# Kernel tuning notes

Measured on AMD Instinct MI355X. Metric: run time of the kernel, lower is better.

Reference implementation:

```python
import jax, jax.numpy as jnp
import numpy as np

GROUPS = 32
EPS = 1e-6


def group_norm(x, scale, bias):
    # x: [b,h,w,c] channels-last, 32 groups
    b, h, w, c = x.shape
    g = GROUPS
    xg = x.reshape(b, h, w, g, c // g)
    mean = xg.mean(axis=(1, 2, 4), keepdims=True)
    var = xg.var(axis=(1, 2, 4), keepdims=True)
    xg = (xg - mean) * jax.lax.rsqrt(var + EPS)
    return xg.reshape(b, h, w, c) * scale + bias


def setup_inputs() -> dict:
    key = jax.random.key(0)
    ks = jax.random.split(key, 10)
    b, h, w, c = 8, 64, 64, 256
    x = jax.random.normal(ks[0], (b, h, w, c), dtype=jnp.float32)
    s = 1.0 / np.sqrt(c)
    return {
        "x": x,
        "gn_scale": jnp.ones((c,), jnp.float32),
        "gn_bias": jnp.zeros((c,), jnp.float32),
        "wq": jax.random.normal(ks[1], (c, c), jnp.float32) * s,
        "bq": jnp.zeros((c,), jnp.float32),
        "wk": jax.random.normal(ks[2], (c, c), jnp.float32) * s,
        "bk": jnp.zeros((c,), jnp.float32),
        "wv": jax.random.normal(ks[3], (c, c), jnp.float32) * s,
        "bv": jnp.zeros((c,), jnp.float32),
        "wp": jax.random.normal(ks[4], (c, c), jnp.float32) * s,
        "bp": jnp.zeros((c,), jnp.float32),
    }


def reference(x, gn_scale, gn_bias, wq, bq, wk, bk, wv, bv, wp, bp):
    b, h, w, c = x.shape
    h_ = group_norm(x, gn_scale, gn_bias)
    # 1x1 convs == per-pixel channel matmuls
    q = jnp.einsum('bhwc,cd->bhwd', h_, wq) + bq
    k = jnp.einsum('bhwc,cd->bhwd', h_, wk) + bk
    v = jnp.einsum('bhwc,cd->bhwd', h_, wv) + bv
    q = q.reshape(b, h * w, c)
    k = k.reshape(b, h * w, c)
    v = v.reshape(b, h * w, c)
    scores = jnp.einsum('bqc,bkc->bqk', q, k) * (c ** -0.5)  # [b, hw, hw]
    attn = jax.nn.softmax(scores, axis=2)
    out = jnp.einsum('bqk,bkc->bqc', attn, v).reshape(b, h, w, c)
    out = jnp.einsum('bhwc,cd->bhwd', out, wp) + bp
    return x + out
```

## Files before the change

kernel.cpp:

```cpp
#include <hip/hip_runtime.h>
#include <hip/hip_bf16.h>
#include <stdint.h>

static constexpr int HW = 4096;
static constexpr int Cc = 256;
static constexpr int Gg = 32;
static constexpr float EPSV = 1e-6f;
static constexpr float QSCALE = 0.0625f * 1.44269504f;

typedef __attribute__((ext_vector_type(8))) short bf8_t;
typedef __attribute__((ext_vector_type(4))) float f4_t;
typedef __attribute__((ext_vector_type(16))) float f32x16;

__device__ __forceinline__ ushort f2bf(float x) {
    union { float f; uint32_t u; } v; v.f = x;
    uint32_t r = v.u + 0x7FFFu + ((v.u >> 16) & 1u);
    return (ushort)(r >> 16);
}
__device__ __forceinline__ float bf2f(ushort u) {
    union { uint32_t u; float f; } v; v.u = ((uint32_t)u) << 16;
    return v.f;
}
__device__ __forceinline__ uint32_t cvtpk(float lo, float hi_) {
    uint32_t r;
    asm volatile("v_cvt_pk_bf16_f32 %0, %1, %2" : "=v"(r) : "v"(lo), "v"(hi_));
    return r;
}
__device__ __forceinline__ float fexp2(float x) {
    float r;
    asm("v_exp_f32 %0, %1" : "=v"(r) : "v"(x));
    return r;
}

__device__ __forceinline__ void gload16(const void* g, void* l) {
    __builtin_amdgcn_global_load_lds((const __attribute__((address_space(1))) void*)g,
                                     (__attribute__((address_space(3))) void*)l, 16, 0, 0);
}

__global__ void prep_kernel(const float* __restrict__ x, float* __restrict__ psum,
                            float* __restrict__ psumsq,
                            const float* __restrict__ wq, const float* __restrict__ wk,
                            const float* __restrict__ wv, const float* __restrict__ wp,
                            ushort* __restrict__ wT) {
    int bx = blockIdx.x;
    if (bx < 512) {
        int slice = bx & 63;
        int b = bx >> 6;
        int c = threadIdx.x;
        const float* xp = x + ((size_t)b * HW + (size_t)slice * 64) * Cc + c;
        float s = 0.f, sq = 0.f;
        for (int p = 0; p < 64; ++p) { float v = xp[(size_t)p * Cc]; s += v; sq += v * v; }
        for (int m = 1; m < 8; m <<= 1) { s += __shfl_xor(s, m); sq += __shfl_xor(sq, m); }
        if ((c & 7) == 0) {
            int g = c >> 3;
            psum[(b * Gg + g) * 64 + slice] = s;
            psumsq[(b * Gg + g) * 64 + slice] = sq;
        }
    } else {
        int base = (bx - 512) * 1024 + threadIdx.x * 4;
        int which = base >> 16;
        const float* w = which == 0 ? wq : which == 1 ? wk : which == 2 ? wv : wp;
        int rem = base & 65535;
        int d = rem >> 8, c = rem & 255;
        ushort4 o;
        o.x = f2bf(w[(c + 0) * 256 + d]);
        o.y = f2bf(w[(c + 1) * 256 + d]);
        o.z = f2bf(w[(c + 2) * 256 + d]);
        o.w = f2bf(w[(c + 3) * 256 + d]);
        *(ushort4*)&wT[which * 65536 + d * 256 + c] = o;
    }
}

__global__ void gn_stats(const float* __restrict__ psum, const float* __restrict__ psumsq,
                         float* __restrict__ stats) {
    int t = threadIdx.x;
    float s = 0.f, sq = 0.f;
    for (int i = 0; i < 64; ++i) { s += psum[t * 64 + i]; sq += psumsq[t * 64 + i]; }
    float mean = s * (1.0f / 32768.0f);
    float var = sq * (1.0f / 32768.0f) - mean * mean;
    stats[t * 2] = mean;
    stats[t * 2 + 1] = rsqrtf(var + EPSV);
}

__global__ __launch_bounds__(256) void qkv_gn(const float* __restrict__ x, const float* __restrict__ stats,
                                              const float* __restrict__ gs, const float* __restrict__ gb,
                                              const ushort* __restrict__ wT,
                                              const float* __restrict__ bq, const float* __restrict__ bk,
                                              const float* __restrict__ bv,
                                              ushort* __restrict__ q, ushort* __restrict__ k,
                                              ushort* __restrict__ vT) {
    int lane = threadIdx.x & 63, wvi = threadIdx.x >> 6;
    int lq = lane & 15, lg = lane >> 4;
    int nf0 = wvi * 4;
    int m0b = blockIdx.x * 64;

    bf8_t a[4][8];
#pragma unroll
    for (int tt = 0; tt < 4; ++tt) {
        int row = m0b + tt * 16 + lq;
        int batch = row >> 12;
        const float* xr = x + (size_t)row * 256;
#pragma unroll
        for (int ks = 0; ks < 8; ++ks) {
            int c0 = ks * 32 + lg * 8;
            int g = c0 >> 3;
            float2 st = *(const float2*)&stats[(batch * Gg + g) * 2];
            float4 v0 = *(const float4*)&xr[c0];
            float4 v1 = *(const float4*)&xr[c0 + 4];
            float4 s0 = *(const float4*)&gs[c0];
            float4 s1 = *(const float4*)&gs[c0 + 4];
            float4 b0 = *(const float4*)&gb[c0];
            float4 b1 = *(const float4*)&gb[c0 + 4];
            bf8_t fr;
            fr[0] = (short)f2bf((v0.x - st.x) * st.y * s0.x + b0.x);
            fr[1] = (short)f2bf((v0.y - st.x) * st.y * s0.y + b0.y);
            fr[2] = (short)f2bf((v0.z - st.x) * st.y * s0.z + b0.z);
            fr[3] = (short)f2bf((v0.w - st.x) * st.y * s0.w + b0.w);
            fr[4] = (short)f2bf((v1.x - st.x) * st.y * s1.x + b1.x);
            fr[5] = (short)f2bf((v1.y - st.x) * st.y * s1.y + b1.y);
            fr[6] = (short)f2bf((v1.z - st.x) * st.y * s1.z + b1.z);
            fr[7] = (short)f2bf((v1.w - st.x) * st.y * s1.w + b1.w);
            a[tt][ks] = fr;
        }
    }

#pragma unroll
    for (int which = 0; which < 3; ++which) {
        const ushort* w = wT + which * 65536;
        const float* bias = which == 0 ? bq : which == 1 ? bk : bv;

        f4_t acc[4][4];
#pragma unroll
        for (int tt = 0; tt < 4; ++tt)
#pragma unroll
            for (int i = 0; i < 4; ++i) acc[tt][i] = (f4_t)0.f;

        const ushort* brow = w + (size_t)(nf0 * 16 + lq) * 256 + lg * 8;
#pragma unroll
        for (int nf = 0; nf < 4; ++nf) {
#pragma unroll
            for (int ks = 0; ks < 8; ++ks) {
                bf8_t bfr = *(const bf8_t*)(brow + nf * 16 * 256 + ks * 32);
                acc[0][nf] = __builtin_amdgcn_mfma_f32_16x16x32_bf16(a[0][ks], bfr, acc[0][nf], 0, 0, 0);
                acc[1][nf] = __builtin_amdgcn_mfma_f32_16x16x32_bf16(a[1][ks], bfr, acc[1][nf], 0, 0, 0);
                acc[2][nf] = __builtin_amdgcn_mfma_f32_16x16x32_bf16(a[2][ks], bfr, acc[2][nf], 0, 0, 0);
                acc[3][nf] = __builtin_amdgcn_mfma_f32_16x16x32_bf16(a[3][ks], bfr, acc[3][nf], 0, 0, 0);
            }
        }
#pragma unroll
        for (int tt = 0; tt < 4; ++tt) {
            int m0 = m0b + tt * 16;
            if (which == 2) {
                int bt = m0 >> 12;
                int hw0 = (m0 & 4095) + lg * 4;
#pragma unroll
                for (int nf = 0; nf < 4; ++nf) {
                    int col = (nf0 + nf) * 16 + lq;
                    float bsv = bias[col];
                    ushort4 pk;
                    pk.x = f2bf(acc[tt][nf][0] + bsv);
                    pk.y = f2bf(acc[tt][nf][1] + bsv);
                    pk.z = f2bf(acc[tt][nf][2] + bsv);
                    pk.w = f2bf(acc[tt][nf][3] + bsv);
                    *(ushort4*)&vT[(size_t)bt * (256 * 4096) + (size_t)col * 4096 + hw0] = pk;
                }
            } else {
                ushort* out = which == 0 ? q : k;
                float scale = which == 0 ? QSCALE : 1.0f;
#pragma unroll
                for (int nf = 0; nf < 4; ++nf) {
                    int col = (nf0 + nf) * 16 + lq;
                    float bsv = bias[col];
#pragma unroll
                    for (int r = 0; r < 4; ++r) {
                        int rr = m0 + lg * 4 + r;
                        out[(size_t)rr * 256 + col] = f2bf((acc[tt][nf][r] + bsv) * scale);
                    }
                }
            }
        }
    }
}

__global__ __launch_bounds__(512, 2) void flash_kernel(const ushort* __restrict__ q,
                                                       const ushort* __restrict__ kk,
                                                       const ushort* __restrict__ vT,
                                                       ushort* __restrict__ Opart,
                                                       float* __restrict__ ml) {
    extern __shared__ char smem[];
    const int t = threadIdx.x, lane = t & 63, wvi = t >> 6;
    const int l31 = lane & 31, hi = lane >> 5;
    const int bid = blockIdx.x;
    const int batch = bid & 7, half = (bid >> 3) & 1, qt = bid >> 4;
    const size_t bb = (size_t)batch * HW * Cc;
    const int t0 = half * 32;

    const int qbase = qt * 256 + wvi * 32;
    bf8_t qf[16];
    {
        const ushort* qrow = q + bb + (size_t)(qbase + l31) * Cc + hi * 8;
#pragma unroll
        for (int ks = 0; ks < 16; ++ks) qf[ks] = *(const bf8_t*)(qrow + ks * 16);
    }

    f32x16 o[8];
#pragma unroll
    for (int i = 0; i < 8; ++i) o[i] = (f32x16)0.f;
    float l_i = 0.f;

    const ushort* ksrc_b = kk + bb;
    const ushort* vsrc_b = vT + (size_t)batch * (256 * 4096);
    const int tb = wvi * 64;

    auto stage = [&](int kt, int bufsel) {
        const ushort* ks_ = ksrc_b + (size_t)kt * 64 * 256;
        const ushort* vs_ = vsrc_b + kt * 64;
        char* kd = smem + bufsel * 32768;
        char* vd = smem + 65536 + bufsel * 32768;
#pragma unroll
        for (int i = 0; i < 4; ++i) {
            int n = i * 512 + tb + lane;
            int kr = n >> 5;
            int c = (n & 31) ^ (kr & 7);
            gload16(ks_ + kr * 256 + c * 8, kd + (i * 512 + tb) * 16);
        }
#pragma unroll
        for (int i = 0; i < 4; ++i) {
            int n = i * 512 + tb + lane;
            int d = n >> 3;
            int c = (n & 7) ^ (d & 7);
            gload16(vs_ + (size_t)d * HW + c * 8, vd + (i * 512 + tb) * 16);
        }
    };

    stage(t0, 0);
    asm volatile("s_waitcnt vmcnt(0)" ::: "memory");
    __builtin_amdgcn_s_barrier();
    __builtin_amdgcn_sched_barrier(0);

    for (int it = 0; it < 32; ++it) {
        const int cur = it & 1;
        if (it + 1 < 32) stage(t0 + it + 1, cur ^ 1);

        const char* Kb = smem + cur * 32768;
        const char* Vb = smem + 65536 + cur * 32768;

        f32x16 sa0 = (f32x16)(-8.0f), sa1 = (f32x16)(-8.0f);
        __builtin_amdgcn_s_setprio(1);
#pragma unroll
        for (int ks = 0; ks < 16; ++ks) {
            int chunk = 2 * ks + hi;
            int sw = (chunk ^ (l31 & 7)) * 16;
            bf8_t kf0 = *(const bf8_t*)(Kb + l31 * 512 + sw);
            bf8_t kf1 = *(const bf8_t*)(Kb + (32 + l31) * 512 + sw);
            sa0 = __builtin_amdgcn_mfma_f32_32x32x16_bf16(kf0, qf[ks], sa0, 0, 0, 0);
            sa1 = __builtin_amdgcn_mfma_f32_32x32x16_bf16(kf1, qf[ks], sa1, 0, 0, 0);
        }
        __builtin_amdgcn_s_setprio(0);

#pragma unroll
        for (int s = 0; s < 4; ++s) {
            int b8 = (s & 1) * 8;
            float p0, p1, p2, p3, p4, p5, p6, p7;
            if (s < 2) {
                p0 = fexp2(sa0[b8 + 0]); p1 = fexp2(sa0[b8 + 1]);
                p2 = fexp2(sa0[b8 + 2]); p3 = fexp2(sa0[b8 + 3]);
                p4 = fexp2(sa0[b8 + 4]); p5 = fexp2(sa0[b8 + 5]);
                p6 = fexp2(sa0[b8 + 6]); p7 = fexp2(sa0[b8 + 7]);
            } else {
                p0 = fexp2(sa1[b8 + 0]); p1 = fexp2(sa1[b8 + 1]);
                p2 = fexp2(sa1[b8 + 2]); p3 = fexp2(sa1[b8 + 3]);
                p4 = fexp2(sa1[b8 + 4]); p5 = fexp2(sa1[b8 + 5]);
                p6 = fexp2(sa1[b8 + 6]); p7 = fexp2(sa1[b8 + 7]);
            }
            l_i += ((p0 + p1) + (p2 + p3)) + ((p4 + p5) + (p6 + p7));
            uint32_t w0 = cvtpk(p0, p1), w1 = cvtpk(p2, p3);
            uint32_t w2 = cvtpk(p4, p5), w3 = cvtpk(p6, p7);
            asm volatile("v_permlane32_swap_b32 %0, %1" : "+v"(w0), "+v"(w2));
            asm volatile("v_permlane32_swap_b32 %0, %1" : "+v"(w1), "+v"(w3));
            union { uint32_t u[4]; bf8_t v; } pa;
            pa.u[0] = w0; pa.u[1] = w1; pa.u[2] = w2; pa.u[3] = w3;

            __builtin_amdgcn_s_setprio(1);
#pragma unroll
            for (int nt = 0; nt < 8; ++nt) {
                int d = nt * 32 + l31;
                int ch = 2 * s + hi;
                bf8_t vf = *(const bf8_t*)(Vb + d * 128 + ((ch ^ (d & 7)) * 16));
                o[nt] = __builtin_amdgcn_mfma_f32_32x32x16_bf16(pa.v, vf, o[nt], 0, 0, 0);
            }
            __builtin_amdgcn_s_setprio(0);
        }

        if (it + 1 < 32) {
            asm volatile("s_waitcnt vmcnt(0)" ::: "memory");
            __builtin_amdgcn_s_barrier();
            __builtin_amdgcn_sched_barrier(0);
        }
    }

    float l_row = l_i + __shfl_xor(l_i, 32);
    ushort* op = Opart + (size_t)bid * (256 * 256) + (size_t)(wvi * 32) * 256;
#pragma unroll
    for (int nt = 0; nt < 8; ++nt) {
#pragma unroll
        for (int r = 0; r < 16; ++r) {
            int qrow = (r & 3) + 8 * (r >> 2) + 4 * hi;
            op[(size_t)qrow * 256 + nt * 32 + l31] = f2bf(o[nt][r]);
        }
    }
    if (lane < 32) {
        ml[(size_t)bid * 256 + wvi * 32 + l31] = l_row;
    }
}

__global__ __launch_bounds__(256) void projc_gemm(const ushort* __restrict__ Opart,
                                                  const float* __restrict__ ml,
                                                  const ushort* __restrict__ wT,
                                                  const float* __restrict__ bp,
                                                  const float* __restrict__ x,
                                                  float* __restrict__ outp) {
    int lane = threadIdx.x & 63, wvi = threadIdx.x >> 6;
    int lq = lane & 15, lg = lane >> 4;
    int rowhalf = wvi >> 1, nf0 = (wvi & 1) * 8;
    int m0b = blockIdx.x * 64 + rowhalf * 32;

    bf8_t a[2][8];
#pragma unroll
    for (int tt = 0; tt < 2; ++tt) {
        int row = m0b + tt * 16 + lq;
        int batch = row >> 12, rr = row & 4095;
        int qt = rr >> 8, rit = rr & 255;
        int blkA = batch + 16 * qt, blkB = blkA + 8;
        float la = ml[(size_t)blkA * 256 + rit];
        float lb = ml[(size_t)blkB * 256 + rit];
        float inv = 1.0f / (la + lb);
        const ushort* Arow = Opart + (size_t)blkA * 65536 + (size_t)rit * 256 + lg * 8;
        const ushort* Brow = Opart + (size_t)blkB * 65536 + (size_t)rit * 256 + lg * 8;
#pragma unroll
        for (int ks = 0; ks < 8; ++ks) {
            bf8_t fa = *(const bf8_t*)(Arow + ks * 32);
            bf8_t fb = *(const bf8_t*)(Brow + ks * 32);
            bf8_t mg;
#pragma unroll
            for (int j = 0; j < 8; ++j)
                mg[j] = (short)f2bf((bf2f((ushort)fa[j]) + bf2f((ushort)fb[j])) * inv);
            a[tt][ks] = mg;
        }
    }

    f4_t acc[2][8];
#pragma unroll
    for (int tt = 0; tt < 2; ++tt)
#pragma unroll
        for (int i = 0; i < 8; ++i) acc[tt][i] = (f4_t)0.f;

    const ushort* brow = wT + (size_t)(nf0 * 16 + lq) * 256 + lg * 8;
#pragma unroll
    for (int nf = 0; nf < 8; ++nf) {
#pragma unroll
        for (int ks = 0; ks < 8; ++ks) {
            bf8_t bfr = *(const bf8_t*)(brow + nf * 16 * 256 + ks * 32);
            acc[0][nf] = __builtin_amdgcn_mfma_f32_16x16x32_bf16(a[0][ks], bfr, acc[0][nf], 0, 0, 0);
            acc[1][nf] = __builtin_amdgcn_mfma_f32_16x16x32_bf16(a[1][ks], bfr, acc[1][nf], 0, 0, 0);
        }
    }
#pragma unroll
    for (int tt = 0; tt < 2; ++tt) {
#pragma unroll
        for (int nf = 0; nf < 8; ++nf) {
            int col = (nf0 + nf) * 16 + lq;
            float bsv = bp[col];
#pragma unroll
            for (int r = 0; r < 4; ++r) {
                size_t idx = (size_t)(m0b + tt * 16 + lg * 4 + r) * 256 + col;
                outp[idx] = x[idx] + acc[tt][nf][r] + bsv;
            }
        }
    }
}

extern "C" void kernel_launch(void* const* d_in, const int* in_sizes, int n_in,
                              void* d_out, int out_size, void* d_ws, size_t ws_size,
                              hipStream_t stream) {
    const float* x  = (const float*)d_in[0];
    const float* gs = (const float*)d_in[1];
    const float* gb = (const float*)d_in[2];
    const float* wq = (const float*)d_in[3];
    const float* bq = (const float*)d_in[4];
    const float* wk = (const float*)d_in[5];
    const float* bk = (const float*)d_in[6];
    const float* wv = (const float*)d_in[7];
    const float* bv = (const float*)d_in[8];
    const float* wp = (const float*)d_in[9];
    const float* bp = (const float*)d_in[10];
    float* out = (float*)d_out;

    char* ws = (char*)d_ws;
    ushort* wT    = (ushort*)ws;
    float*  psum  = (float*)(ws + 512 * 1024);
    float*  psumsq= (float*)(ws + 576 * 1024);
    float*  stats = (float*)(ws + 640 * 1024);
    ushort* qb    = (ushort*)(ws + (size_t)17 * (1 << 20));
    ushort* kb    = (ushort*)(ws + (size_t)33 * (1 << 20));
    ushort* vTb   = (ushort*)(ws + (size_t)49 * (1 << 20));
    ushort* Opart = (ushort*)(ws + (size_t)65 * (1 << 20));
    float*  mlb   = (float*)(ws + (size_t)97 * (1 << 20));

    prep_kernel<<<768, 256, 0, stream>>>(x, psum, psumsq, wq, wk, wv, wp, wT);
    gn_stats<<<1, 256, 0, stream>>>(psum, psumsq, stats);
    qkv_gn<<<512, 256, 0, stream>>>(x, stats, gs, gb, wT, bq, bk, bv, qb, kb, vTb);

    hipFuncSetAttribute(reinterpret_cast<const void*>(flash_kernel),
                        hipFuncAttributeMaxDynamicSharedMemorySize, 131072);
    flash_kernel<<<256, 512, 131072, stream>>>(qb, kb, vTb, Opart, mlb);

    projc_gemm<<<512, 256, 0, stream>>>(Opart, mlb, wT + 3 * 65536, bp, x, out);
}
```

Measured before the change: 257.7 us.

## Shrink flash attention tiles to 128 query rows and 32-key stages

Restructures the flash kernel from 512-thread blocks with 256 query rows and 64-key tiles to 256-thread blocks with 128 query rows and 32-key tiles. The grid doubles to 512 blocks and LDS per block halves to 64KB, so more blocks can be resident per CU and the grid covers the device more evenly. The LDS swizzles and the projection kernel's indexing change to match the new partial-output layout. In exchange each K/V tile is reused by fewer query rows, so global and LDS traffic grows, and twice as many loop iterations each pay a barrier.

Result: no change. 253.0 us (-1.9%).

```diff
diff --git a/kernel.cpp b/kernel.cpp
--- a/kernel.cpp
+++ b/kernel.cpp
@@ -182,7 +182,7 @@
     }
 }
 
-__global__ __launch_bounds__(512, 2) void flash_kernel(const ushort* __restrict__ q,
+__global__ __launch_bounds__(256, 2) void flash_kernel(const ushort* __restrict__ q,
                                                        const ushort* __restrict__ kk,
                                                        const ushort* __restrict__ vT,
                                                        ushort* __restrict__ Opart,
@@ -193,9 +193,9 @@
     const int bid = blockIdx.x;
     const int batch = bid & 7, half = (bid >> 3) & 1, qt = bid >> 4;
     const size_t bb = (size_t)batch * HW * Cc;
-    const int t0 = half * 32;
-
-    const int qbase = qt * 256 + wvi * 32;
+    const int t0 = half * 64;
+
+    const int qbase = qt * 128 + wvi * 32;
     bf8_t qf[16];
     {
         const ushort* qrow = q + bb + (size_t)(qbase + l31) * Cc + hi * 8;
@@ -210,26 +210,25 @@
 
     const ushort* ksrc_b = kk + bb;
     const ushort* vsrc_b = vT + (size_t)batch * (256 * 4096);
-    const int tb = wvi * 64;
 
     auto stage = [&](int kt, int bufsel) {
-        const ushort* ks_ = ksrc_b + (size_t)kt * 64 * 256;
-        const ushort* vs_ = vsrc_b + kt * 64;
-        char* kd = smem + bufsel * 32768;
-        char* vd = smem + 65536 + bufsel * 32768;
+        const ushort* ks_ = ksrc_b + (size_t)kt * 32 * 256;
+        const ushort* vs_ = vsrc_b + kt * 32;
+        char* kd = smem + bufsel * 16384;
+        char* vd = smem + 32768 + bufsel * 16384;
 #pragma unroll
         for (int i = 0; i < 4; ++i) {
-            int n = i * 512 + tb + lane;
+            int n = i * 256 + t;
             int kr = n >> 5;
             int c = (n & 31) ^ (kr & 7);
-            gload16(ks_ + kr * 256 + c * 8, kd + (i * 512 + tb) * 16);
+            gload16(ks_ + kr * 256 + c * 8, kd + n * 16);
         }
 #pragma unroll
         for (int i = 0; i < 4; ++i) {
-            int n = i * 512 + tb + lane;
-            int d = n >> 3;
-            int c = (n & 7) ^ (d & 7);
-            gload16(vs_ + (size_t)d * HW + c * 8, vd + (i * 512 + tb) * 16);
+            int n = i * 256 + t;
+            int d = n >> 2;
+            int c = (n & 3) ^ (d & 3);
+            gload16(vs_ + (size_t)d * HW + c * 8, vd + n * 16);
         }
     };
 
@@ -238,41 +237,31 @@
     __builtin_amdgcn_s_barrier();
     __builtin_amdgcn_sched_barrier(0);
 
-    for (int it = 0; it < 32; ++it) {
+    for (int it = 0; it < 64; ++it) {
         const int cur = it & 1;
-        if (it + 1 < 32) stage(t0 + it + 1, cur ^ 1);
-
-        const char* Kb = smem + cur * 32768;
-        const char* Vb = smem + 65536 + cur * 32768;
-
-        f32x16 sa0 = (f32x16)(-8.0f), sa1 = (f32x16)(-8.0f);
+        if (it + 1 < 64) stage(t0 + it + 1, cur ^ 1);
+
+        const char* Kb = smem + cur * 16384;
+        const char* Vb = smem + 32768 + cur * 16384;
+
+        f32x16 sa = (f32x16)(-8.0f);
         __builtin_amdgcn_s_setprio(1);
 #pragma unroll
         for (int ks = 0; ks < 16; ++ks) {
             int chunk = 2 * ks + hi;
             int sw = (chunk ^ (l31 & 7)) * 16;
-            bf8_t kf0 = *(const bf8_t*)(Kb + l31 * 512 + sw);
-            bf8_t kf1 = *(const bf8_t*)(Kb + (32 + l31) * 512 + sw);
-            sa0 = __builtin_amdgcn_mfma_f32_32x32x16_bf16(kf0, qf[ks], sa0, 0, 0, 0);
-            sa1 = __builtin_amdgcn_mfma_f32_32x32x16_bf16(kf1, qf[ks], sa1, 0, 0, 0);
+            bf8_t kf = *(const bf8_t*)(Kb + l31 * 512 + sw);
+            sa = __builtin_amdgcn_mfma_f32_32x32x16_bf16(kf, qf[ks], sa, 0, 0, 0);
         }
         __builtin_amdgcn_s_setprio(0);
 
 #pragma unroll
-        for (int s = 0; s < 4; ++s) {
-            int b8 = (s & 1) * 8;
-            float p0, p1, p2, p3, p4, p5, p6, p7;
-            if (s < 2) {
-                p0 = fexp2(sa0[b8 + 0]); p1 = fexp2(sa0[b8 + 1]);
-                p2 = fexp2(sa0[b8 + 2]); p3 = fexp2(sa0[b8 + 3]);
-                p4 = fexp2(sa0[b8 + 4]); p5 = fexp2(sa0[b8 + 5]);
-                p6 = fexp2(sa0[b8 + 6]); p7 = fexp2(sa0[b8 + 7]);
-            } else {
-                p0 = fexp2(sa1[b8 + 0]); p1 = fexp2(sa1[b8 + 1]);
-                p2 = fexp2(sa1[b8 + 2]); p3 = fexp2(sa1[b8 + 3]);
-                p4 = fexp2(sa1[b8 + 4]); p5 = fexp2(sa1[b8 + 5]);
-                p6 = fexp2(sa1[b8 + 6]); p7 = fexp2(sa1[b8 + 7]);
-            }
+        for (int s = 0; s < 2; ++s) {
+            int b8 = s * 8;
+            float p0 = fexp2(sa[b8 + 0]), p1 = fexp2(sa[b8 + 1]);
+            float p2 = fexp2(sa[b8 + 2]), p3 = fexp2(sa[b8 + 3]);
+            float p4 = fexp2(sa[b8 + 4]), p5 = fexp2(sa[b8 + 5]);
+            float p6 = fexp2(sa[b8 + 6]), p7 = fexp2(sa[b8 + 7]);
             l_i += ((p0 + p1) + (p2 + p3)) + ((p4 + p5) + (p6 + p7));
             uint32_t w0 = cvtpk(p0, p1), w1 = cvtpk(p2, p3);
             uint32_t w2 = cvtpk(p4, p5), w3 = cvtpk(p6, p7);
@@ -286,13 +275,13 @@
             for (int nt = 0; nt < 8; ++nt) {
                 int d = nt * 32 + l31;
                 int ch = 2 * s + hi;
-                bf8_t vf = *(const bf8_t*)(Vb + d * 128 + ((ch ^ (d & 7)) * 16));
+                bf8_t vf = *(const bf8_t*)(Vb + d * 64 + ((ch ^ (d & 3)) * 16));
                 o[nt] = __builtin_amdgcn_mfma_f32_32x32x16_bf16(pa.v, vf, o[nt], 0, 0, 0);
             }
             __builtin_amdgcn_s_setprio(0);
         }
 
-        if (it + 1 < 32) {
+        if (it + 1 < 64) {
             asm volatile("s_waitcnt vmcnt(0)" ::: "memory");
             __builtin_amdgcn_s_barrier();
             __builtin_amdgcn_sched_barrier(0);
@@ -300,7 +289,7 @@
     }
 
     float l_row = l_i + __shfl_xor(l_i, 32);
-    ushort* op = Opart + (size_t)bid * (256 * 256) + (size_t)(wvi * 32) * 256;
+    ushort* op = Opart + (size_t)bid * (128 * 256) + (size_t)(wvi * 32) * 256;
 #pragma unroll
     for (int nt = 0; nt < 8; ++nt) {
 #pragma unroll
@@ -310,7 +299,7 @@
         }
     }
     if (lane < 32) {
-        ml[(size_t)bid * 256 + wvi * 32 + l31] = l_row;
+        ml[(size_t)bid * 128 + wvi * 32 + l31] = l_row;
     }
 }
 
@@ -330,13 +319,13 @@
     for (int tt = 0; tt < 2; ++tt) {
         int row = m0b + tt * 16 + lq;
         int batch = row >> 12, rr = row & 4095;
-        int qt = rr >> 8, rit = rr & 255;
+        int qt = rr >> 7, rit = rr & 127;
         int blkA = batch + 16 * qt, blkB = blkA + 8;
-        float la = ml[(size_t)blkA * 256 + rit];
-        float lb = ml[(size_t)blkB * 256 + rit];
+        float la = ml[(size_t)blkA * 128 + rit];
+        float lb = ml[(size_t)blkB * 128 + rit];
         float inv = 1.0f / (la + lb);
-        const ushort* Arow = Opart + (size_t)blkA * 65536 + (size_t)rit * 256 + lg * 8;
-        const ushort* Brow = Opart + (size_t)blkB * 65536 + (size_t)rit * 256 + lg * 8;
+        const ushort* Arow = Opart + (size_t)blkA * 32768 + (size_t)rit * 256 + lg * 8;
+        const ushort* Brow = Opart + (size_t)blkB * 32768 + (size_t)rit * 256 + lg * 8;
 #pragma unroll
         for (int ks = 0; ks < 8; ++ks) {
             bf8_t fa = *(const bf8_t*)(Arow + ks * 32);
@@ -412,8 +401,8 @@
     qkv_gn<<<512, 256, 0, stream>>>(x, stats, gs, gb, wT, bq, bk, bv, qb, kb, vTb);
 
     hipFuncSetAttribute(reinterpret_cast<const void*>(flash_kernel),
-                        hipFuncAttributeMaxDynamicSharedMemorySize, 131072);
-    flash_kernel<<<256, 512, 131072, stream>>>(qb, kb, vTb, Opart, mlb);
+                        hipFuncAttributeMaxDynamicSharedMemorySize, 65536);
+    flash_kernel<<<512, 256, 65536, stream>>>(qb, kb, vTb, Opart, mlb);
 
     projc_gemm<<<512, 256, 0, stream>>>(Opart, mlb, wT + 3 * 65536, bp, x, out);
 }
```
